# Kernel optimization log

Hardware: AMD Instinct MI355X
Metric: run time of the kernel (lower is better)

The kernel has to match this reference:

```python
import jax, jax.numpy as jnp
import numpy as np

SIGMA = 1.0
ALPHA = 64.0
EPS = 1e-8


def setup_inputs() -> dict:
    key = jax.random.key(0)
    z = jax.random.normal(key, (8192, 1024), dtype=jnp.float32)
    return {"z": z}


def reference(z):
    # L2 normalize rows (matches F.normalize(p=2, dim=1))
    z = z / jnp.maximum(jnp.linalg.norm(z, axis=1, keepdims=True), 1e-12)
    N = z.shape[0] // 2
    z1, z2 = z[:N], z[N:]

    inv2s2 = 1.0 / (2.0 * SIGMA ** 2)

    # positive pairs: squared distance between aligned rows
    d_pos = jnp.sum((z1 - z2) ** 2, axis=1)              # [N]
    g_pos = jnp.exp(-d_pos * inv2s2)
    s_pos = jnp.log(g_pos + EPS) + 1.0                    # f' for KL

    # negative pairs: full NxN squared euclidean distance on z1
    sq = jnp.sum(z1 * z1, axis=1)                         # [N]
    d2 = sq[:, None] + sq[None, :] - 2.0 * (z1 @ z1.T)    # [N, N]
    d2 = jnp.maximum(d2, 0.0)
    g_neg = jnp.exp(-d2 * inv2s2)
    s_neg = jnp.log(g_neg + EPS) + 1.0
    star_neg = jnp.exp(s_neg - 1.0)                       # f* for KL

    # masked mean over off-diagonal entries
    offdiag = ~jnp.eye(N, dtype=bool)
    star_mean = jnp.sum(jnp.where(offdiag, star_neg, 0.0)) / (N * (N - 1))

    loss = -jnp.mean(s_pos) + ALPHA * star_mean
    return loss
```

## Files before the change

### kernel.cpp

```cpp
#include <hip/hip_runtime.h>
#include <hip/hip_bf16.h>
#include <stdint.h>


#define AS1 __attribute__((address_space(1)))
#define AS3 __attribute__((address_space(3)))

typedef unsigned short u16;
typedef uint8_t  u8;
typedef int    i32x4 __attribute__((ext_vector_type(4)));
typedef int    i32x8 __attribute__((ext_vector_type(8)));
typedef float  f32x4 __attribute__((ext_vector_type(4)));

constexpr int   D     = 1024;
constexpr int   N     = 4096;
constexpr int   TM    = 128;
constexpr int   BK    = 128;
constexpr int   NB    = N / TM;
constexpr int   NTRI  = NB * (NB + 1) / 2;
constexpr float EPS   = 1e-8f;
constexpr float ALPHA = 64.0f;

__device__ __forceinline__ void async_load16(const void* g, void* l) {
    __builtin_amdgcn_global_load_lds((AS1 void*)g, (AS3 void*)l, 16, 0, 0);
}

__global__ __launch_bounds__(256) void norm_spos_kernel(
    const float* __restrict__ z, u8* __restrict__ q, float* __restrict__ spos)
{
    const int row = blockIdx.x;
    const int t   = threadIdx.x;
    const int lane = t & 63, wave = t >> 6;

    const float4 a = ((const float4*)(z + (size_t)row       * D))[t];
    const float4 b = ((const float4*)(z + (size_t)(row + N) * D))[t];

    float s1 = a.x*a.x + a.y*a.y + a.z*a.z + a.w*a.w;
    float s2 = b.x*b.x + b.y*b.y + b.z*b.z + b.w*b.w;
    #pragma unroll
    for (int off = 32; off; off >>= 1) {
        s1 += __shfl_down(s1, off);
        s2 += __shfl_down(s2, off);
    }
    __shared__ float r1[4], r2[4], r3[4];
    if (lane == 0) { r1[wave] = s1; r2[wave] = s2; }
    __syncthreads();
    const float ss1 = r1[0] + r1[1] + r1[2] + r1[3];
    const float ss2 = r2[0] + r2[1] + r2[2] + r2[3];
    const float inv1 = 1.0f / fmaxf(sqrtf(ss1), 1e-12f);
    const float inv2 = 1.0f / fmaxf(sqrtf(ss2), 1e-12f);

    float4 an, bn;
    an.x = a.x * inv1; an.y = a.y * inv1; an.z = a.z * inv1; an.w = a.w * inv1;
    bn.x = b.x * inv2; bn.y = b.y * inv2; bn.z = b.z * inv2; bn.w = b.w * inv2;

    int u = __builtin_amdgcn_cvt_pk_fp8_f32(an.x, an.y, 0, false);
    u     = __builtin_amdgcn_cvt_pk_fp8_f32(an.z, an.w, u, true);
    ((int*)(q + (size_t)row * D))[t] = u;

    const float dx = an.x - bn.x, dy = an.y - bn.y, dz = an.z - bn.z, dw = an.w - bn.w;
    float dp = dx*dx + dy*dy + dz*dz + dw*dw;
    #pragma unroll
    for (int off = 32; off; off >>= 1) dp += __shfl_down(dp, off);
    if (lane == 0) r3[wave] = dp;
    __syncthreads();
    if (t == 0) {
        const float d_pos = r3[0] + r3[1] + r3[2] + r3[3];
        const float g     = expf(-0.5f * d_pos);
        spos[row] = logf(g + EPS) + 1.0f;
    }
}

__global__ __launch_bounds__(256) void gram_kernel(
    const u8* __restrict__ Q, float* __restrict__ star_part)
{
    __shared__ __align__(16) u8 lA[TM * BK];
    __shared__ __align__(16) u8 lB[TM * BK];
    __shared__ float wsum[4];

    int bi = 0, rem = blockIdx.x;
    while (rem >= NB - bi) { rem -= NB - bi; ++bi; }
    const int bj    = bi + rem;
    const int rowA0 = bi * TM, rowB0 = bj * TM;
    const bool diag = (bi == bj);

    const int t    = threadIdx.x;
    const int lane = t & 63;
    const int wave = t >> 6;
    const int wm   = (wave & 1) * 64;
    const int wn   = (wave >> 1) * 64;
    const int fr   = lane & 15;
    const int fq   = lane >> 4;

    const u8* gA[4]; const u8* gB[4]; u8* dA[4]; u8* dB[4];
    #pragma unroll
    for (int j = 0; j < 4; ++j) {
        const int p = t + 256 * j;
        const int r = p >> 3;
        const int c = (p & 7) ^ (r & 7);
        gA[j] = Q + (size_t)(rowA0 + r) * D + c * 16;
        gB[j] = Q + (size_t)(rowB0 + r) * D + c * 16;
        dA[j] = &lA[p * 16];
        dB[j] = &lB[p * 16];
    }

    f32x4 acc[4][4];
    #pragma unroll
    for (int mt = 0; mt < 4; ++mt)
        #pragma unroll
        for (int nt = 0; nt < 4; ++nt)
            acc[mt][nt] = f32x4{0.f, 0.f, 0.f, 0.f};

    for (int k0 = 0; k0 < D; k0 += BK) {
        #pragma unroll
        for (int j = 0; j < 4; ++j) {
            async_load16(gA[j] + k0, dA[j]);
            async_load16(gB[j] + k0, dB[j]);
        }
        __syncthreads();

        i32x8 af[4], bf[4];
        #pragma unroll
        for (int mt = 0; mt < 4; ++mt) {
            const int r = wm + mt * 16 + fr;
            const i32x4* base = (const i32x4*)&lA[r * BK];
            const i32x4 lo = base[(2 * fq    ) ^ (r & 7)];
            const i32x4 hi = base[(2 * fq + 1) ^ (r & 7)];
            af[mt][0] = lo[0]; af[mt][1] = lo[1]; af[mt][2] = lo[2]; af[mt][3] = lo[3];
            af[mt][4] = hi[0]; af[mt][5] = hi[1]; af[mt][6] = hi[2]; af[mt][7] = hi[3];
        }
        #pragma unroll
        for (int nt = 0; nt < 4; ++nt) {
            const int r = wn + nt * 16 + fr;
            const i32x4* base = (const i32x4*)&lB[r * BK];
            const i32x4 lo = base[(2 * fq    ) ^ (r & 7)];
            const i32x4 hi = base[(2 * fq + 1) ^ (r & 7)];
            bf[nt][0] = lo[0]; bf[nt][1] = lo[1]; bf[nt][2] = lo[2]; bf[nt][3] = lo[3];
            bf[nt][4] = hi[0]; bf[nt][5] = hi[1]; bf[nt][6] = hi[2]; bf[nt][7] = hi[3];
        }

        #pragma unroll
        for (int mt = 0; mt < 4; ++mt)
            #pragma unroll
            for (int nt = 0; nt < 4; ++nt)
                acc[mt][nt] = __builtin_amdgcn_mfma_scale_f32_16x16x128_f8f6f4(
                    af[mt], bf[nt], acc[mt][nt],
                    0, 0,
                    0, 0x7f7f7f7f,
                    0, 0x7f7f7f7f);

        __syncthreads();
    }

    float lsum = 0.0f;
    #pragma unroll
    for (int mt = 0; mt < 4; ++mt) {
        #pragma unroll
        for (int nt = 0; nt < 4; ++nt) {
            #pragma unroll
            for (int r = 0; r < 4; ++r) {
                const float g  = acc[mt][nt][r];
                const int   gi = wm + mt * 16 + fq * 4 + r;
                const int   gj = wn + nt * 16 + fr;
                const float d2 = fmaxf(2.0f - 2.0f * g, 0.0f);
                const float e  = __expf(-0.5f * d2);
                lsum += (diag && gi == gj) ? 0.0f : e;
            }
        }
    }
    #pragma unroll
    for (int off = 32; off; off >>= 1) lsum += __shfl_down(lsum, off);
    if (lane == 0) wsum[wave] = lsum;
    __syncthreads();
    if (t == 0)
        star_part[blockIdx.x] = (diag ? 1.0f : 2.0f) *
                                (wsum[0] + wsum[1] + wsum[2] + wsum[3]);
}

__global__ __launch_bounds__(256) void finalize_kernel(
    const float* __restrict__ spos, const float* __restrict__ star,
    float* __restrict__ out)
{
    const int t = threadIdx.x, lane = t & 63, wave = t >> 6;
    float s1 = 0.0f, s2 = 0.0f;
    for (int i = t; i < N;    i += 256) s1 += spos[i];
    for (int i = t; i < NTRI; i += 256) s2 += star[i];
    #pragma unroll
    for (int off = 32; off; off >>= 1) {
        s1 += __shfl_down(s1, off);
        s2 += __shfl_down(s2, off);
    }
    __shared__ float r1[4], r2[4];
    if (lane == 0) { r1[wave] = s1; r2[wave] = s2; }
    __syncthreads();
    if (t == 0) {
        const float spos_sum = r1[0] + r1[1] + r1[2] + r1[3];
        const float star_sum = r2[0] + r2[1] + r2[2] + r2[3];
        const float star_mean = star_sum / ((float)N * (float)(N - 1)) + EPS;
        out[0] = -spos_sum / (float)N + ALPHA * star_mean;
    }
}

extern "C" void kernel_launch(void* const* d_in, const int* in_sizes, int n_in,
                              void* d_out, int out_size, void* d_ws, size_t ws_size,
                              hipStream_t stream)
{
    (void)in_sizes; (void)n_in; (void)out_size; (void)ws_size;
    const float* z    = (const float*)d_in[0];
    float*       out  = (float*)d_out;
    u8*          q    = (u8*)d_ws;
    float*       spos = (float*)((char*)d_ws + (size_t)N * D);
    float*       star = spos + N;

    hipLaunchKernelGGL(norm_spos_kernel, dim3(N),    dim3(256), 0, stream, z, q, spos);
    hipLaunchKernelGGL(gram_kernel,      dim3(NTRI), dim3(256), 0, stream, q, star);
    hipLaunchKernelGGL(finalize_kernel,  dim3(1),    dim3(256), 0, stream, spos, star, out);
}
```

Baseline: 98.14 us.

## Make gram kernel persistent with atomic work-stealing over triangular tiles

The gram kernel now launches a fixed grid of 512 blocks instead of one block per upper-triangular tile. Each block loops, taking its next tile index from a global atomic counter that the normalization kernel resets, and keeps a running weighted sum that is written once per block. The intent is to balance the 528 tiles across CUs and cut the tail effect of a second partial wave. The cost is a global atomic plus an extra barrier per tile, and the partial-sum buffer shrinks to 512 entries.

```diff
diff --git a/kernel.cpp b/kernel.cpp
--- a/kernel.cpp
+++ b/kernel.cpp
@@ -18,6 +18,7 @@
 constexpr int   BK    = 128;
 constexpr int   NB    = N / TM;
 constexpr int   NTRI  = NB * (NB + 1) / 2;
+constexpr int   GBLK  = 512;
 constexpr float EPS   = 1e-8f;
 constexpr float ALPHA = 64.0f;
 
@@ -26,11 +27,14 @@
 }
 
 __global__ __launch_bounds__(256) void norm_spos_kernel(
-    const float* __restrict__ z, u8* __restrict__ q, float* __restrict__ spos)
+    const float* __restrict__ z, u8* __restrict__ q, float* __restrict__ spos,
+    int* __restrict__ ctr)
 {
     const int row = blockIdx.x;
     const int t   = threadIdx.x;
     const int lane = t & 63, wave = t >> 6;
+
+    if (row == 0 && t == 0) *ctr = GBLK;
 
     const float4 a = ((const float4*)(z + (size_t)row       * D))[t];
     const float4 b = ((const float4*)(z + (size_t)(row + N) * D))[t];
@@ -72,17 +76,12 @@
 }
 
 __global__ __launch_bounds__(256) void gram_kernel(
-    const u8* __restrict__ Q, float* __restrict__ star_part)
+    const u8* __restrict__ Q, float* __restrict__ star_part, int* __restrict__ ctr)
 {
     __shared__ __align__(16) u8 lA[TM * BK];
     __shared__ __align__(16) u8 lB[TM * BK];
     __shared__ float wsum[4];
-
-    int bi = 0, rem = blockIdx.x;
-    while (rem >= NB - bi) { rem -= NB - bi; ++bi; }
-    const int bj    = bi + rem;
-    const int rowA0 = bi * TM, rowB0 = bj * TM;
-    const bool diag = (bi == bj);
+    __shared__ int   nxt;
 
     const int t    = threadIdx.x;
     const int lane = t & 63;
@@ -92,89 +91,104 @@
     const int fr   = lane & 15;
     const int fq   = lane >> 4;
 
-    const u8* gA[4]; const u8* gB[4]; u8* dA[4]; u8* dB[4];
+    int   ro[4], co[4];
     #pragma unroll
     for (int j = 0; j < 4; ++j) {
         const int p = t + 256 * j;
-        const int r = p >> 3;
-        const int c = (p & 7) ^ (r & 7);
-        gA[j] = Q + (size_t)(rowA0 + r) * D + c * 16;
-        gB[j] = Q + (size_t)(rowB0 + r) * D + c * 16;
-        dA[j] = &lA[p * 16];
-        dB[j] = &lB[p * 16];
-    }
-
-    f32x4 acc[4][4];
-    #pragma unroll
-    for (int mt = 0; mt < 4; ++mt)
+        ro[j] = p >> 3;
+        co[j] = ((p & 7) ^ (ro[j] & 7)) * 16;
+    }
+
+    float bsum = 0.0f;
+
+    for (int tile = blockIdx.x; tile < NTRI; ) {
+        int bi = 0, rem = tile;
+        while (rem >= NB - bi) { rem -= NB - bi; ++bi; }
+        const int bj    = bi + rem;
+        const int rowA0 = bi * TM, rowB0 = bj * TM;
+        const bool diag = (bi == bj);
+        const u8* QA = Q + (size_t)rowA0 * D;
+        const u8* QB = Q + (size_t)rowB0 * D;
+
+        f32x4 acc[4][4];
         #pragma unroll
-        for (int nt = 0; nt < 4; ++nt)
-            acc[mt][nt] = f32x4{0.f, 0.f, 0.f, 0.f};
-
-    for (int k0 = 0; k0 < D; k0 += BK) {
-        #pragma unroll
-        for (int j = 0; j < 4; ++j) {
-            async_load16(gA[j] + k0, dA[j]);
-            async_load16(gB[j] + k0, dB[j]);
+        for (int mt = 0; mt < 4; ++mt)
+            #pragma unroll
+            for (int nt = 0; nt < 4; ++nt)
+                acc[mt][nt] = f32x4{0.f, 0.f, 0.f, 0.f};
+
+        for (int k0 = 0; k0 < D; k0 += BK) {
+            #pragma unroll
+            for (int j = 0; j < 4; ++j) {
+                const size_t go = (size_t)ro[j] * D + k0 + co[j];
+                async_load16(QA + go, &lA[(t + 256 * j) * 16]);
+                async_load16(QB + go, &lB[(t + 256 * j) * 16]);
+            }
+            __syncthreads();
+
+            i32x8 af[4], bf[4];
+            #pragma unroll
+            for (int mt = 0; mt < 4; ++mt) {
+                const int r = wm + mt * 16 + fr;
+                const i32x4* base = (const i32x4*)&lA[r * BK];
+                const i32x4 lo = base[(2 * fq    ) ^ (r & 7)];
+                const i32x4 hi = base[(2 * fq + 1) ^ (r & 7)];
+                af[mt][0] = lo[0]; af[mt][1] = lo[1]; af[mt][2] = lo[2]; af[mt][3] = lo[3];
+                af[mt][4] = hi[0]; af[mt][5] = hi[1]; af[mt][6] = hi[2]; af[mt][7] = hi[3];
+            }
+            #pragma unroll
+            for (int nt = 0; nt < 4; ++nt) {
+                const int r = wn + nt * 16 + fr;
+                const i32x4* base = (const i32x4*)&lB[r * BK];
+                const i32x4 lo = base[(2 * fq    ) ^ (r & 7)];
+                const i32x4 hi = base[(2 * fq + 1) ^ (r & 7)];
+                bf[nt][0] = lo[0]; bf[nt][1] = lo[1]; bf[nt][2] = lo[2]; bf[nt][3] = lo[3];
+                bf[nt][4] = hi[0]; bf[nt][5] = hi[1]; bf[nt][6] = hi[2]; bf[nt][7] = hi[3];
+            }
+
+            #pragma unroll
+            for (int mt = 0; mt < 4; ++mt)
+                #pragma unroll
+                for (int nt = 0; nt < 4; ++nt)
+                    acc[mt][nt] = __builtin_amdgcn_mfma_scale_f32_16x16x128_f8f6f4(
+                        af[mt], bf[nt], acc[mt][nt],
+                        0, 0,
+                        0, 0x7f7f7f7f,
+                        0, 0x7f7f7f7f);
+
+            __syncthreads();
         }
-        __syncthreads();
-
-        i32x8 af[4], bf[4];
+
+        const float w = diag ? 1.0f : 2.0f;
+        float tsum = 0.0f;
         #pragma unroll
         for (int mt = 0; mt < 4; ++mt) {
-            const int r = wm + mt * 16 + fr;
-            const i32x4* base = (const i32x4*)&lA[r * BK];
-            const i32x4 lo = base[(2 * fq    ) ^ (r & 7)];
-            const i32x4 hi = base[(2 * fq + 1) ^ (r & 7)];
-            af[mt][0] = lo[0]; af[mt][1] = lo[1]; af[mt][2] = lo[2]; af[mt][3] = lo[3];
-            af[mt][4] = hi[0]; af[mt][5] = hi[1]; af[mt][6] = hi[2]; af[mt][7] = hi[3];
+            #pragma unroll
+            for (int nt = 0; nt < 4; ++nt) {
+                #pragma unroll
+                for (int r = 0; r < 4; ++r) {
+                    const float g  = acc[mt][nt][r];
+                    const int   gi = wm + mt * 16 + fq * 4 + r;
+                    const int   gj = wn + nt * 16 + fr;
+                    const float d2 = fmaxf(2.0f - 2.0f * g, 0.0f);
+                    const float e  = __expf(-0.5f * d2);
+                    tsum += (diag && gi == gj) ? 0.0f : e;
+                }
+            }
         }
-        #pragma unroll
-        for (int nt = 0; nt < 4; ++nt) {
-            const int r = wn + nt * 16 + fr;
-            const i32x4* base = (const i32x4*)&lB[r * BK];
-            const i32x4 lo = base[(2 * fq    ) ^ (r & 7)];
-            const i32x4 hi = base[(2 * fq + 1) ^ (r & 7)];
-            bf[nt][0] = lo[0]; bf[nt][1] = lo[1]; bf[nt][2] = lo[2]; bf[nt][3] = lo[3];
-            bf[nt][4] = hi[0]; bf[nt][5] = hi[1]; bf[nt][6] = hi[2]; bf[nt][7] = hi[3];
-        }
-
-        #pragma unroll
-        for (int mt = 0; mt < 4; ++mt)
-            #pragma unroll
-            for (int nt = 0; nt < 4; ++nt)
-                acc[mt][nt] = __builtin_amdgcn_mfma_scale_f32_16x16x128_f8f6f4(
-                    af[mt], bf[nt], acc[mt][nt],
-                    0, 0,
-                    0, 0x7f7f7f7f,
-                    0, 0x7f7f7f7f);
-
+        bsum += w * tsum;
+
+        if (t == 0) nxt = atomicAdd(ctr, 1);
         __syncthreads();
-    }
-
-    float lsum = 0.0f;
-    #pragma unroll
-    for (int mt = 0; mt < 4; ++mt) {
-        #pragma unroll
-        for (int nt = 0; nt < 4; ++nt) {
-            #pragma unroll
-            for (int r = 0; r < 4; ++r) {
-                const float g  = acc[mt][nt][r];
-                const int   gi = wm + mt * 16 + fq * 4 + r;
-                const int   gj = wn + nt * 16 + fr;
-                const float d2 = fmaxf(2.0f - 2.0f * g, 0.0f);
-                const float e  = __expf(-0.5f * d2);
-                lsum += (diag && gi == gj) ? 0.0f : e;
-            }
-        }
-    }
-    #pragma unroll
-    for (int off = 32; off; off >>= 1) lsum += __shfl_down(lsum, off);
-    if (lane == 0) wsum[wave] = lsum;
+        tile = nxt;
+    }
+
+    #pragma unroll
+    for (int off = 32; off; off >>= 1) bsum += __shfl_down(bsum, off);
+    if (lane == 0) wsum[wave] = bsum;
     __syncthreads();
     if (t == 0)
-        star_part[blockIdx.x] = (diag ? 1.0f : 2.0f) *
-                                (wsum[0] + wsum[1] + wsum[2] + wsum[3]);
+        star_part[blockIdx.x] = wsum[0] + wsum[1] + wsum[2] + wsum[3];
 }
 
 __global__ __launch_bounds__(256) void finalize_kernel(
@@ -184,7 +198,7 @@
     const int t = threadIdx.x, lane = t & 63, wave = t >> 6;
     float s1 = 0.0f, s2 = 0.0f;
     for (int i = t; i < N;    i += 256) s1 += spos[i];
-    for (int i = t; i < NTRI; i += 256) s2 += star[i];
+    for (int i = t; i < GBLK; i += 256) s2 += star[i];
     #pragma unroll
     for (int off = 32; off; off >>= 1) {
         s1 += __shfl_down(s1, off);
@@ -211,8 +225,9 @@
     u8*          q    = (u8*)d_ws;
     float*       spos = (float*)((char*)d_ws + (size_t)N * D);
     float*       star = spos + N;
-
-    hipLaunchKernelGGL(norm_spos_kernel, dim3(N),    dim3(256), 0, stream, z, q, spos);
-    hipLaunchKernelGGL(gram_kernel,      dim3(NTRI), dim3(256), 0, stream, q, star);
+    int*         ctr  = (int*)(star + GBLK);
+
+    hipLaunchKernelGGL(norm_spos_kernel, dim3(N),    dim3(256), 0, stream, z, q, spos, ctr);
+    hipLaunchKernelGGL(gram_kernel,      dim3(GBLK), dim3(256), 0, stream, q, star, ctr);
     hipLaunchKernelGGL(finalize_kernel,  dim3(1),    dim3(256), 0, stream, spos, star, out);
 }
```

Measured after the change: 121.4 us. +23.7%, slower.
